# Kernel tuning notes

Measured on AMD Instinct MI355X. Metric: run time of the kernel, lower is better.

## Reference

```python
import jax, jax.numpy as jnp
import numpy as np

EMBED_DIM = 1024
NUM_HEADS = 16
HEAD_DIM = EMBED_DIM // NUM_HEADS
SCALE = HEAD_DIM ** -0.5


def setup_inputs() -> dict:
    key = jax.random.key(0)
    k1, k2, k3, k4 = jax.random.split(key, 4)
    B, N, C = 4, 2048, EMBED_DIM
    x = jax.random.normal(k1, (B, N, C), dtype=jnp.float32)
    # qkv: Linear(C, 3C, bias=False)
    w_qkv = jax.random.normal(k2, (3 * C, C), dtype=jnp.float32) * (C ** -0.5)
    # proj: Linear(C, C, bias=True)
    w_proj = jax.random.normal(k3, (C, C), dtype=jnp.float32) * (C ** -0.5)
    b_proj = jax.random.normal(k4, (C,), dtype=jnp.float32) * 0.01
    return {"x": x, "w_qkv": w_qkv, "w_proj": w_proj, "b_proj": b_proj}


def reference(x, w_qkv, w_proj, b_proj):
    B, N, C = x.shape
    H, D = NUM_HEADS, HEAD_DIM
    qkv = jnp.einsum('bnc,oc->bno', x, w_qkv)               # [B,N,3C]
    qkv = qkv.reshape(B, N, 3, H, D).transpose(2, 0, 3, 1, 4)  # [3,B,H,N,D]
    q, k, v = qkv[0], qkv[1], qkv[2]
    attn = jnp.einsum('bhnd,bhmd->bhnm', q, k) * SCALE       # [B,H,N,N]
    attn = jax.nn.softmax(attn, axis=-1)
    out = jnp.einsum('bhnm,bhmd->bhnd', attn, v)             # [B,H,N,D]
    out = out.transpose(0, 2, 1, 3).reshape(B, N, C)
    return jnp.einsum('bnc,oc->bno', out, w_proj) + b_proj
```

## Files before the change

kernel.cpp:

```cpp
#include <hip/hip_runtime.h>

#define B_ 4
#define N_ 2048
#define C_ 1024
#define H_ 16
#define D_ 64
#define M_ (B_*N_)

typedef _Float16 f16;
typedef __attribute__((ext_vector_type(2))) _Float16 f16x2;
typedef __attribute__((ext_vector_type(4))) _Float16 f16x4;
typedef __attribute__((ext_vector_type(8))) _Float16 f16x8;
typedef __attribute__((ext_vector_type(4))) float f32x4;
typedef __attribute__((ext_vector_type(16))) float f32x16;
typedef unsigned int u32;
typedef __attribute__((ext_vector_type(2))) u32 u32x2;
typedef __attribute__((ext_vector_type(4))) u32 u32x4;

__device__ __forceinline__ f32x4 mfma16(f16x8 a, f16x8 b, f32x4 c) {
  return __builtin_amdgcn_mfma_f32_16x16x32_f16(a, b, c, 0, 0, 0);
}
__device__ __forceinline__ f32x16 mfma32(f16x8 a, f16x8 b, f32x16 c) {
  return __builtin_amdgcn_mfma_f32_32x32x16_f16(a, b, c, 0, 0, 0);
}

__global__ void cast_f32_f16(const float* __restrict__ in, f16* __restrict__ out,
                             int n4, int scale_n4, float scale) {
  int i = blockIdx.x * blockDim.x + threadIdx.x;
  int stride = gridDim.x * blockDim.x;
  for (; i < n4; i += stride) {
    float4 v = reinterpret_cast<const float4*>(in)[i];
    float s = (i < scale_n4) ? scale : 1.0f;
    f16x4 o = { (f16)(v.x*s), (f16)(v.y*s), (f16)(v.z*s), (f16)(v.w*s) };
    reinterpret_cast<f16x4*>(out)[i] = o;
  }
}

template<int OUTMODE>
__global__ __launch_bounds__(256) void gemm_bt(
    const f16* __restrict__ A, const f16* __restrict__ Bm,
    f16* __restrict__ outH, float* __restrict__ outF,
    const float* __restrict__ bias, int M, int Nn, int K)
{
  __shared__ __align__(16) f16 As[128*32];
  __shared__ __align__(16) f16 Bs[128*32];
  const int tid = threadIdx.x;
  const int lane = tid & 63, wid = tid >> 6;
  const int wr = wid >> 1, wc = wid & 1;
  const int g = lane >> 4, r15 = lane & 15;
  const int nbx = Nn >> 7;
  const int cpx = gridDim.x >> 3;
  const int wg = blockIdx.x;
  const int swz = (wg & 7) * cpx + (wg >> 3);
  const int m0 = (swz / nbx) * 128, n0 = (swz % nbx) * 128;

  f32x4 acc[4][4] = {};

  for (int k0 = 0; k0 < K; k0 += 32) {
#pragma unroll
    for (int i = 0; i < 2; ++i) {
      int chunk = wid*128 + i*64 + lane;
      int row = chunk >> 2, c8 = (chunk & 3) << 3;
      const f16* ga = A  + (size_t)(m0 + row) * K + k0 + c8;
      const f16* gb = Bm + (size_t)(n0 + row) * K + k0 + c8;
      __builtin_amdgcn_global_load_lds(
        (const __attribute__((address_space(1))) unsigned int*)ga,
        (__attribute__((address_space(3))) unsigned int*)&As[(wid*128 + i*64)*8], 16, 0, 0);
      __builtin_amdgcn_global_load_lds(
        (const __attribute__((address_space(1))) unsigned int*)gb,
        (__attribute__((address_space(3))) unsigned int*)&Bs[(wid*128 + i*64)*8], 16, 0, 0);
    }
    __syncthreads();

    f16x8 af[4], bfr[4];
#pragma unroll
    for (int m = 0; m < 4; ++m)
      af[m] = *reinterpret_cast<const f16x8*>(&As[(wr*64 + m*16 + r15)*32 + g*8]);
#pragma unroll
    for (int n = 0; n < 4; ++n)
      bfr[n] = *reinterpret_cast<const f16x8*>(&Bs[(wc*64 + n*16 + r15)*32 + g*8]);
#pragma unroll
    for (int m = 0; m < 4; ++m)
#pragma unroll
      for (int n = 0; n < 4; ++n)
        acc[m][n] = mfma16(af[m], bfr[n], acc[m][n]);
    __syncthreads();
  }

#pragma unroll
  for (int m = 0; m < 4; ++m) {
#pragma unroll
    for (int n = 0; n < 4; ++n) {
#pragma unroll
      for (int r = 0; r < 4; ++r) {
        int row = m0 + wr*64 + m*16 + g*4 + r;
        int col = n0 + wc*64 + n*16 + r15;
        if (OUTMODE == 0) {
          outH[(size_t)row * Nn + col] = (f16)acc[m][n][r];
        } else {
          outF[(size_t)row * Nn + col] = acc[m][n][r] + bias[col];
        }
      }
    }
  }
}

__global__ __launch_bounds__(256) void transpose_v(const f16* __restrict__ qkv,
                                                   f16* __restrict__ vt) {
  __shared__ f16 Ts[64*64];
  const int tid = threadIdx.x;
  const int bh = blockIdx.y, b = bh >> 4, h = bh & 15;
  const int n0 = blockIdx.x * 64;
#pragma unroll
  for (int p = 0; p < 2; ++p) {
    int idx = p*256 + tid;
    int row = idx >> 3, c8 = (idx & 7) << 3;
    f16x8 v = *reinterpret_cast<const f16x8*>(
        qkv + (size_t)(b*N_ + n0 + row)*(3*C_) + 2*C_ + h*D_ + c8);
    *reinterpret_cast<f16x8*>(&Ts[row*64 + c8]) = v;
  }
  __syncthreads();
#pragma unroll
  for (int p = 0; p < 2; ++p) {
    int idx = p*256 + tid;
    int d = idx & 63, cblk = idx >> 6;
    f16x8 o;
#pragma unroll
    for (int j = 0; j < 8; ++j) o[j] = Ts[(cblk*8 + j)*64 + d];
    *reinterpret_cast<f16x8*>(vt + (size_t)(bh*64 + d)*N_ + n0 + cblk*8) = o;
  }
}

__global__ __launch_bounds__(256, 3) void attn_kernel(
    const f16* __restrict__ qkv, const f16* __restrict__ vt,
    f16* __restrict__ attn_out)
{
  __shared__ __align__(16) f16 Ks[2][64*64];
  __shared__ __align__(16) f16 Vs[2][64*64];
  const int tid = threadIdx.x;
  const int lane = tid & 63, w = tid >> 6;
  const int hi = lane >> 5;
  const int r31 = lane & 31;
  const int rm = r31 & 7;
  const int blk = blockIdx.x;
  const int xcd = blk & 7, idx = blk >> 3;
  const int bh = xcd + 8 * (idx >> 4);
  const int bx = idx & 15;
  const int b = bh >> 4, h = bh & 15;
  const int q0 = bx * 128 + w * 32;
  const int RS = 3 * C_;

  f16x8 qf[4];
  {
    const f16* qrow = qkv + (size_t)(b*N_ + q0 + r31) * RS + h*D_;
#pragma unroll
    for (int kk = 0; kk < 4; ++kk)
      qf[kk] = *reinterpret_cast<const f16x8*>(qrow + kk*16 + hi*8);
  }

  f32x16 acc0 = {}, acc1 = {};
  const f32x16 Zc = {};
  const f16x2 one2 = { (f16)1.0f, (f16)1.0f };
  float la = 0.f, lb = 0.f;

  int cc0 = w*64 + lane, cc1 = 256 + w*64 + lane;
  int R0 = cc0 >> 3, s0_ = (cc0 & 7) ^ (R0 & 7);
  int R1 = cc1 >> 3, s1_ = (cc1 & 7) ^ (R1 & 7);
  const f16* kg0 = qkv + (size_t)(b*N_ + R0) * RS + C_ + h*D_ + s0_*8;
  const f16* kg1 = qkv + (size_t)(b*N_ + R1) * RS + C_ + h*D_ + s1_*8;
  const f16* vg0 = vt + (size_t)(bh*D_ + R0) * N_ + s0_*8;
  const f16* vg1 = vt + (size_t)(bh*D_ + R1) * N_ + s1_*8;

  auto stage = [&](int bufi, int kv0) {
    __builtin_amdgcn_global_load_lds(
      (const __attribute__((address_space(1))) u32*)(kg0 + (size_t)kv0 * RS),
      (__attribute__((address_space(3))) u32*)&Ks[bufi][(w*64)*8], 16, 0, 0);
    __builtin_amdgcn_global_load_lds(
      (const __attribute__((address_space(1))) u32*)(kg1 + (size_t)kv0 * RS),
      (__attribute__((address_space(3))) u32*)&Ks[bufi][(256 + w*64)*8], 16, 0, 0);
    __builtin_amdgcn_global_load_lds(
      (const __attribute__((address_space(1))) u32*)(vg0 + kv0),
      (__attribute__((address_space(3))) u32*)&Vs[bufi][(w*64)*8], 16, 0, 0);
    __builtin_amdgcn_global_load_lds(
      (const __attribute__((address_space(1))) u32*)(vg1 + kv0),
      (__attribute__((address_space(3))) u32*)&Vs[bufi][(256 + w*64)*8], 16, 0, 0);
  };

  int cur = 0;
  stage(0, 0);
  __syncthreads();

  for (int it = 0; it < N_/64; ++it) {
    if (it + 1 < N_/64) stage(cur ^ 1, (it + 1) * 64);
    const f16* KsC = Ks[cur];
    const f16* VsC = Vs[cur];

    f32x16 T0, T1;
    __builtin_amdgcn_s_setprio(1);
    {
      int ch = ((hi ^ rm) << 3);
      f16x8 k0 = *reinterpret_cast<const f16x8*>(&KsC[r31*64 + ch]);
      f16x8 k1 = *reinterpret_cast<const f16x8*>(&KsC[(32 + r31)*64 + ch]);
      T0 = mfma32(k0, qf[0], Zc);
      T1 = mfma32(k1, qf[0], Zc);
    }
#pragma unroll
    for (int kk = 1; kk < 4; ++kk) {
      int ch = (((kk*2 + hi) ^ rm) << 3);
      f16x8 k0 = *reinterpret_cast<const f16x8*>(&KsC[r31*64 + ch]);
      f16x8 k1 = *reinterpret_cast<const f16x8*>(&KsC[(32 + r31)*64 + ch]);
      T0 = mfma32(k0, qf[kk], T0);
      T1 = mfma32(k1, qf[kk], T1);
    }
    __builtin_amdgcn_s_setprio(0);

    u32 wpk[16];
#pragma unroll
    for (int i = 0; i < 8; ++i) {
      float p0 = __builtin_amdgcn_exp2f(T0[2*i]);
      float p1 = __builtin_amdgcn_exp2f(T0[2*i+1]);
      u32 pk = __builtin_bit_cast(u32, __builtin_amdgcn_cvt_pkrtz(p0, p1));
      wpk[i] = pk;
      la = __builtin_amdgcn_fdot2(__builtin_bit_cast(f16x2, pk), one2, la, false);
    }
#pragma unroll
    for (int i = 0; i < 8; ++i) {
      float p0 = __builtin_amdgcn_exp2f(T1[2*i]);
      float p1 = __builtin_amdgcn_exp2f(T1[2*i+1]);
      u32 pk = __builtin_bit_cast(u32, __builtin_amdgcn_cvt_pkrtz(p0, p1));
      wpk[8 + i] = pk;
      lb = __builtin_amdgcn_fdot2(__builtin_bit_cast(f16x2, pk), one2, lb, false);
    }

    __builtin_amdgcn_s_setprio(1);
#pragma unroll
    for (int c = 0; c < 4; ++c) {
      u32x2 r02 = __builtin_amdgcn_permlane32_swap(wpk[4*c],     wpk[4*c + 2], false, false);
      u32x2 r13 = __builtin_amdgcn_permlane32_swap(wpk[4*c + 1], wpk[4*c + 3], false, false);
      u32x4 fw = { r02[0], r13[0], r02[1], r13[1] };
      f16x8 pf = __builtin_bit_cast(f16x8, fw);
      int ch = (((c*2 + hi) ^ rm) << 3);
      f16x8 v0 = *reinterpret_cast<const f16x8*>(&VsC[r31*64 + ch]);
      f16x8 v1 = *reinterpret_cast<const f16x8*>(&VsC[(32 + r31)*64 + ch]);
      acc0 = mfma32(v0, pf, acc0);
      acc1 = mfma32(v1, pf, acc1);
    }
    __builtin_amdgcn_s_setprio(0);

    __syncthreads();
    cur ^= 1;
  }

  float l_own = la + lb;
  float l = l_own + __shfl_xor(l_own, 32);
  float inv = 1.0f / l;
  f16* orow = attn_out + (size_t)(b*N_ + q0 + r31) * C_ + h*D_;
#pragma unroll
  for (int g2 = 0; g2 < 4; ++g2) {
    f16x4 o0, o1;
#pragma unroll
    for (int j = 0; j < 4; ++j) {
      o0[j] = (f16)(acc0[g2*4 + j] * inv);
      o1[j] = (f16)(acc1[g2*4 + j] * inv);
    }
    *reinterpret_cast<f16x4*>(orow + g2*8 + hi*4)      = o0;
    *reinterpret_cast<f16x4*>(orow + 32 + g2*8 + hi*4) = o1;
  }
}

extern "C" void kernel_launch(void* const* d_in, const int* in_sizes, int n_in,
                              void* d_out, int out_size, void* d_ws, size_t ws_size,
                              hipStream_t stream) {
  const float* x      = (const float*)d_in[0];
  const float* w_qkv  = (const float*)d_in[1];
  const float* w_proj = (const float*)d_in[2];
  const float* b_proj = (const float*)d_in[3];
  float* out = (float*)d_out;

  char* ws = (char*)d_ws;
  f16* xb     = (f16*)(ws);
  f16* wqkvb  = (f16*)(ws + 16777216);
  f16* wprojb = (f16*)(ws + 23068672);
  f16* qkvb   = (f16*)(ws + 25165824);
  f16* vtb    = (f16*)(ws + 75497472);
  f16* attnb  = xb;

  cast_f32_f16<<<2048, 256, 0, stream>>>(x,      xb,     (M_*C_)/4, 0, 1.0f);
  cast_f32_f16<<<1024, 256, 0, stream>>>(w_qkv,  wqkvb,  (3*C_*C_)/4, (C_*C_)/4, 0.18033688011112042f);
  cast_f32_f16<<<512,  256, 0, stream>>>(w_proj, wprojb, (C_*C_)/4, 0, 1.0f);

  gemm_bt<0><<<dim3((3*C_/128)*(M_/128)), 256, 0, stream>>>(
      xb, wqkvb, qkvb, nullptr, nullptr, M_, 3*C_, C_);

  transpose_v<<<dim3(N_/64, B_*H_), 256, 0, stream>>>(qkvb, vtb);

  attn_kernel<<<dim3(1024), 256, 0, stream>>>(qkvb, vtb, attnb);

  gemm_bt<1><<<dim3((C_/128)*(M_/128)), 256, 0, stream>>>(
      attnb, wprojb, nullptr, out, b_proj, M_, C_, C_);
}
```

Before: 222.8 us.

## Split QK tile into halves and interleave softmax with PV to raise occupancy

The attention inner loop now computes the score tile in two 32-key halves, doing exp2, packing and PV MFMAs for each half before starting the next. This drops one live f32x16 score accumulator and the 16-word packed buffer, lowering register pressure so launch bounds can ask for 4 waves per SIMD instead of 3. The finer interleaving trades some instruction-level parallelism between the two independent QK chains for more waves to hide latency. The softmax row sums are now split across la/lb differently but still add up to the same total.

```diff
diff --git a/kernel.cpp b/kernel.cpp
--- a/kernel.cpp
+++ b/kernel.cpp
@@ -131,7 +131,7 @@
   }
 }
 
-__global__ __launch_bounds__(256, 3) void attn_kernel(
+__global__ __launch_bounds__(256, 4) void attn_kernel(
     const f16* __restrict__ qkv, const f16* __restrict__ vt,
     f16* __restrict__ attn_out)
 {
@@ -159,7 +159,6 @@
   }
 
   f32x16 acc0 = {}, acc1 = {};
-  const f32x16 Zc = {};
   const f16x2 one2 = { (f16)1.0f, (f16)1.0f };
   float la = 0.f, lb = 0.f;
 
@@ -195,57 +194,58 @@
     const f16* KsC = Ks[cur];
     const f16* VsC = Vs[cur];
 
-    f32x16 T0, T1;
-    __builtin_amdgcn_s_setprio(1);
-    {
-      int ch = ((hi ^ rm) << 3);
-      f16x8 k0 = *reinterpret_cast<const f16x8*>(&KsC[r31*64 + ch]);
-      f16x8 k1 = *reinterpret_cast<const f16x8*>(&KsC[(32 + r31)*64 + ch]);
-      T0 = mfma32(k0, qf[0], Zc);
-      T1 = mfma32(k1, qf[0], Zc);
+#pragma unroll
+    for (int hh = 0; hh < 2; ++hh) {
+      f32x16 T;
+      {
+        const f32x16 Zc = {};
+        __builtin_amdgcn_s_setprio(1);
+        int ch = ((hi ^ rm) << 3);
+        f16x8 k0 = *reinterpret_cast<const f16x8*>(&KsC[(hh*32 + r31)*64 + ch]);
+        T = mfma32(k0, qf[0], Zc);
+#pragma unroll
+        for (int kk = 1; kk < 4; ++kk) {
+          int ch2 = (((kk*2 + hi) ^ rm) << 3);
+          f16x8 kx = *reinterpret_cast<const f16x8*>(&KsC[(hh*32 + r31)*64 + ch2]);
+          T = mfma32(kx, qf[kk], T);
+        }
+        __builtin_amdgcn_s_setprio(0);
+      }
+
+#pragma unroll
+      for (int c2 = 0; c2 < 2; ++c2) {
+        float p0 = __builtin_amdgcn_exp2f(T[8*c2 + 0]);
+        float p1 = __builtin_amdgcn_exp2f(T[8*c2 + 1]);
+        float p2 = __builtin_amdgcn_exp2f(T[8*c2 + 2]);
+        float p3 = __builtin_amdgcn_exp2f(T[8*c2 + 3]);
+        float p4 = __builtin_amdgcn_exp2f(T[8*c2 + 4]);
+        float p5 = __builtin_amdgcn_exp2f(T[8*c2 + 5]);
+        float p6 = __builtin_amdgcn_exp2f(T[8*c2 + 6]);
+        float p7 = __builtin_amdgcn_exp2f(T[8*c2 + 7]);
+        u32 w0 = __builtin_bit_cast(u32, __builtin_amdgcn_cvt_pkrtz(p0, p1));
+        u32 w1 = __builtin_bit_cast(u32, __builtin_amdgcn_cvt_pkrtz(p2, p3));
+        u32 w2 = __builtin_bit_cast(u32, __builtin_amdgcn_cvt_pkrtz(p4, p5));
+        u32 w3 = __builtin_bit_cast(u32, __builtin_amdgcn_cvt_pkrtz(p6, p7));
+        la = __builtin_amdgcn_fdot2(__builtin_bit_cast(f16x2, w0), one2, la, false);
+        lb = __builtin_amdgcn_fdot2(__builtin_bit_cast(f16x2, w1), one2, lb, false);
+        la = __builtin_amdgcn_fdot2(__builtin_bit_cast(f16x2, w2), one2, la, false);
+        lb = __builtin_amdgcn_fdot2(__builtin_bit_cast(f16x2, w3), one2, lb, false);
+
+        u32x2 r02 = __builtin_amdgcn_permlane32_swap(w0, w2, false, false);
+        u32x2 r13 = __builtin_amdgcn_permlane32_swap(w1, w3, false, false);
+        u32x4 fw = { r02[0], r13[0], r02[1], r13[1] };
+        f16x8 pf = __builtin_bit_cast(f16x8, fw);
+
+        int c = hh*2 + c2;
+        int ch = (((c*2 + hi) ^ rm) << 3);
+        f16x8 v0 = *reinterpret_cast<const f16x8*>(&VsC[r31*64 + ch]);
+        f16x8 v1 = *reinterpret_cast<const f16x8*>(&VsC[(32 + r31)*64 + ch]);
+        __builtin_amdgcn_s_setprio(1);
+        acc0 = mfma32(v0, pf, acc0);
+        acc1 = mfma32(v1, pf, acc1);
+        __builtin_amdgcn_s_setprio(0);
+      }
     }
-#pragma unroll
-    for (int kk = 1; kk < 4; ++kk) {
-      int ch = (((kk*2 + hi) ^ rm) << 3);
-      f16x8 k0 = *reinterpret_cast<const f16x8*>(&KsC[r31*64 + ch]);
-      f16x8 k1 = *reinterpret_cast<const f16x8*>(&KsC[(32 + r31)*64 + ch]);
-      T0 = mfma32(k0, qf[kk], T0);
-      T1 = mfma32(k1, qf[kk], T1);
-    }
-    __builtin_amdgcn_s_setprio(0);
-
-    u32 wpk[16];
-#pragma unroll
-    for (int i = 0; i < 8; ++i) {
-      float p0 = __builtin_amdgcn_exp2f(T0[2*i]);
-      float p1 = __builtin_amdgcn_exp2f(T0[2*i+1]);
-      u32 pk = __builtin_bit_cast(u32, __builtin_amdgcn_cvt_pkrtz(p0, p1));
-      wpk[i] = pk;
-      la = __builtin_amdgcn_fdot2(__builtin_bit_cast(f16x2, pk), one2, la, false);
-    }
-#pragma unroll
-    for (int i = 0; i < 8; ++i) {
-      float p0 = __builtin_amdgcn_exp2f(T1[2*i]);
-      float p1 = __builtin_amdgcn_exp2f(T1[2*i+1]);
-      u32 pk = __builtin_bit_cast(u32, __builtin_amdgcn_cvt_pkrtz(p0, p1));
-      wpk[8 + i] = pk;
-      lb = __builtin_amdgcn_fdot2(__builtin_bit_cast(f16x2, pk), one2, lb, false);
-    }
-
-    __builtin_amdgcn_s_setprio(1);
-#pragma unroll
-    for (int c = 0; c < 4; ++c) {
-      u32x2 r02 = __builtin_amdgcn_permlane32_swap(wpk[4*c],     wpk[4*c + 2], false, false);
-      u32x2 r13 = __builtin_amdgcn_permlane32_swap(wpk[4*c + 1], wpk[4*c + 3], false, false);
-      u32x4 fw = { r02[0], r13[0], r02[1], r13[1] };
-      f16x8 pf = __builtin_bit_cast(f16x8, fw);
-      int ch = (((c*2 + hi) ^ rm) << 3);
-      f16x8 v0 = *reinterpret_cast<const f16x8*>(&VsC[r31*64 + ch]);
-      f16x8 v1 = *reinterpret_cast<const f16x8*>(&VsC[(32 + r31)*64 + ch]);
-      acc0 = mfma32(v0, pf, acc0);
-      acc1 = mfma32(v1, pf, acc1);
-    }
-    __builtin_amdgcn_s_setprio(0);
 
     __syncthreads();
     cur ^= 1;
```

Result: no change. 221.8 us (-0.5%).
